# Optimization experiments

Measured on AMD Instinct MI355X. Metric: run time of the kernel, lower is better.

Reference implementation:

```python
import jax, jax.numpy as jnp
import numpy as np

B, T, D, H, C = 32, 512, 1024, 1024, 1000


def setup_inputs() -> dict:
    key = jax.random.key(0)
    ks = jax.random.split(key, 12)
    sc = 0.02
    return {
        "features": jax.random.normal(ks[0], (B, T, D), dtype=jnp.float32),
        "Wp": jax.random.normal(ks[1], (H, D), dtype=jnp.float32) * sc,
        "bp": jnp.zeros((H,), jnp.float32),
        "W_ih": jax.random.normal(ks[2], (3 * H, H), dtype=jnp.float32) * sc,
        "b_ih": jnp.zeros((3 * H,), jnp.float32),
        "W_hh": jax.random.normal(ks[3], (3 * H, H), dtype=jnp.float32) * sc,
        "b_hh": jnp.zeros((3 * H,), jnp.float32),
        "W1": jax.random.normal(ks[4], (H, H), dtype=jnp.float32) * sc,
        "b1": jnp.zeros((H,), jnp.float32),
        "W2": jax.random.normal(ks[5], (C, H), dtype=jnp.float32) * sc,
        "b2": jnp.zeros((C,), jnp.float32),
    }


def _gru_scan(gx, W_hh, b_hh):
    # gx: [B, T, 3H] precomputed input-side gate activations
    def step(h, gx_t):
        gh = h @ W_hh.T + b_hh                  # [B, 3H]
        xr, xz, xn = jnp.split(gx_t, 3, axis=-1)
        hr, hz, hn = jnpp if False else jnp.split(gh, 3, axis=-1)
        r = jax.nn.sigmoid(xr + hr)
        z = jax.nn.sigmoid(xz + hz)
        n = jnp.tanh(xn + r * hn)
        h_new = (1.0 - z) * n + z * h
        return h_new, h_new

    h0 = jnp.zeros((gx.shape[0], W_hh.shape[1]), gx.dtype)
    _, hs = jax.lax.scan(step, h0, jnp.swapaxes(gx, 0, 1))  # [T, B, H]
    return jnp.swapaxes(hs, 0, 1)                            # [B, T, H]


def reference(features, Wp, bp, W_ih, b_ih, W_hh, b_hh, W1, b1, W2, b2):
    # pooled inputs: relu(Linear(features))
    x = jax.nn.relu(jnp.einsum("btd,hd->bth", features, Wp) + bp)  # [B,T,H]
    # input-side gate GEMM batched over all timesteps (the recurrence only
    # needs the hidden-side GEMM per step) -- same math as per-step GRUCell
    gx = jnp.einsum("bth,gh->btg", x, W_ih) + b_ih                 # [B,T,3H]
    hs = _gru_scan(gx, W_hh, b_hh)                                  # [B,T,H]
    out = jax.nn.relu(jnp.einsum("bth,oh->bto", hs, W1) + b1)
    out = jnp.einsum("bth,ch->btc", out, W2) + b2                   # [B,T,C]
    return out
```

## Files before the change

### kernel.cpp

```cpp
#include <hip/hip_runtime.h>
#include <hip/hip_bf16.h>
#include <stdint.h>

#define Bb 32
#define Tt 512
#define Dd 1024
#define Hh 1024
#define Cc 1000
#define Mm (Bb*Tt)
#define SENT 0x7F7F7F7Fu

typedef float f32x4 __attribute__((ext_vector_type(4)));
typedef short bf16x8 __attribute__((ext_vector_type(8)));

#define MFMA16(a,b,c) __builtin_amdgcn_mfma_f32_16x16x32_bf16(a,b,c,0,0,0)

static __device__ __forceinline__ unsigned short f2b(float f){
  __hip_bfloat16 h = __float2bfloat16(f);
  union { __hip_bfloat16 h; unsigned short u; } cv; cv.h = h; return cv.u;
}
static __device__ __forceinline__ float b2f(unsigned short u){
  union { unsigned int i; float f; } cv; cv.i = ((unsigned int)u) << 16; return cv.f;
}

static __device__ __forceinline__ void async16(const ushort* g, ushort* l){
  __builtin_amdgcn_global_load_lds((const __attribute__((address_space(1))) unsigned int*)g,
                                   (__attribute__((address_space(3))) unsigned int*)l,
                                   16, 0, 0);
}

template<int FAST>
static __device__ __forceinline__ bf16x8 h_load(const ushort* p){
  bf16x8 r;
  if constexpr (FAST)
    asm volatile("global_load_dwordx4 %0, %1, off sc1" : "=v"(r) : "v"(p) : "memory");
  else
    asm volatile("global_load_dwordx4 %0, %1, off sc0 sc1" : "=v"(r) : "v"(p) : "memory");
  return r;
}
template<int FAST>
static __device__ __forceinline__ void h_store(ushort* p, unsigned int v){
  if constexpr (FAST)
    asm volatile("global_store_dword %0, %1, off sc1" :: "v"(p), "v"(v) : "memory");
  else
    asm volatile("global_store_dword %0, %1, off sc0 sc1" :: "v"(p), "v"(v) : "memory");
}

static __device__ __forceinline__ int load4sys(const int* p){
  int v;
  asm volatile("global_load_dword %0, %1, off sc0 sc1" : "=v"(v) : "v"(p) : "memory");
  asm volatile("s_waitcnt vmcnt(0)" ::: "memory");
  return v;
}
static __device__ __forceinline__ void store4sys(int* p, int v){
  asm volatile("global_store_dword %0, %1, off sc0 sc1" :: "v"(p), "v"(v) : "memory");
}


__global__ void cvt_bf16(const float* __restrict__ in, ushort* __restrict__ out, int n4){
  int i = blockIdx.x*256 + threadIdx.x;
  if (i < n4){
    const float4 v = ((const float4*)in)[i];
    ushort4 o;
    o.x = f2b(v.x); o.y = f2b(v.y); o.z = f2b(v.z); o.w = f2b(v.w);
    ((ushort4*)out)[i] = o;
  }
}

__global__ void pad_w2(const float* __restrict__ w2, const float* __restrict__ b2,
                       ushort* __restrict__ w2p, float* __restrict__ b2p){
  int i = blockIdx.x*256 + threadIdx.x;
  int r = i >> 10, c = i & 1023;
  w2p[i] = (r < Cc) ? f2b(w2[r*1024 + c]) : (ushort)0;
  if (i < 1024) b2p[i] = (i < Cc) ? b2[i] : 0.f;
}


template<int RELU, int OUT_BF16, int PERM_A, int PERM_C>
__global__ __launch_bounds__(256) void gemm_bt(
    const ushort* __restrict__ A, const ushort* __restrict__ Bm,
    const float* __restrict__ bias, void* __restrict__ Cp,
    int M, int N, int K, int ldc, int nout)
{
  __shared__ ushort As[128*32];
  __shared__ ushort Bs[128*32];
  const int tid  = threadIdx.x;
  const int lane = tid & 63;
  const int wave = tid >> 6;
  const int wr = wave >> 1, wc = wave & 1;
  const int r0 = lane & 15, kg = lane >> 4;

  const int nwg = gridDim.x * gridDim.y;
  const int lin = blockIdx.y * gridDim.x + blockIdx.x;
  const int cpx = nwg >> 3;
  const int swz = (lin & 7) * cpx + (lin >> 3);
  const int bx = swz % gridDim.x, by = swz / gridDim.x;

  const int m0 = bx*128, n0 = by*128;

  const int lrA0 = m0 + (tid>>2);
  const int lrA1 = lrA0 + 64;
  const size_t prA0 = PERM_A ? (size_t)((lrA0 & 511)*32 + (lrA0 >> 9)) : (size_t)lrA0;
  const size_t prA1 = PERM_A ? (size_t)((lrA1 & 511)*32 + (lrA1 >> 9)) : (size_t)lrA1;
  const ushort* aG0 = A  + prA0*K + (tid&3)*8;
  const ushort* aG1 = A  + prA1*K + (tid&3)*8;
  const ushort* bG  = Bm + (size_t)(n0 + (tid>>2))*K + (tid&3)*8;
  ushort* aL = As + tid*8;
  ushort* bL = Bs + tid*8;
  const size_t rstep = (size_t)64*K;

  f32x4 acc[4][4] = {};

  for (int kt = 0; kt < K; kt += 32){
    __syncthreads();
    async16(aG0 + kt, aL);
    async16(aG1 + kt, aL + 2048);
    async16(bG + kt,         bL);
    async16(bG + kt + rstep, bL + 2048);
    __syncthreads();
    bf16x8 af[4], bf_[4];
#pragma unroll
    for (int i=0;i<4;i++) af[i]  = *(const bf16x8*)&As[(wr*64 + i*16 + r0)*32 + kg*8];
#pragma unroll
    for (int j=0;j<4;j++) bf_[j] = *(const bf16x8*)&Bs[(wc*64 + j*16 + r0)*32 + kg*8];
#pragma unroll
    for (int i=0;i<4;i++)
#pragma unroll
      for (int j=0;j<4;j++)
        acc[i][j] = MFMA16(af[i], bf_[j], acc[i][j]);
  }

  const int rowb = m0 + wr*64 + kg*4;
  const int colb = n0 + wc*64 + r0;
#pragma unroll
  for (int i=0;i<4;i++){
#pragma unroll
    for (int j=0;j<4;j++){
      const int c = colb + j*16;
      if (c >= nout) continue;
      const float bv = bias ? bias[c] : 0.f;
#pragma unroll
      for (int q=0;q<4;q++){
        const int r = rowb + i*16 + q;
        const size_t pr = PERM_C ? (size_t)((r & 511)*32 + (r >> 9)) : (size_t)r;
        float v = acc[i][j][q] + bv;
        if (RELU) v = fmaxf(v, 0.f);
        if (OUT_BF16) ((ushort*)Cp)[pr*ldc + c] = f2b(v);
        else          ((float* )Cp)[pr*ldc + c] = v;
      }
    }
  }
}


#define REDN  4656
#define REDN2 1584

template<int FAST>
static __device__ __forceinline__ void scan_body(
    const int g, const int m, const int tid,
    const ushort* __restrict__ Whh, const float* __restrict__ bhh,
    const ushort* __restrict__ W1b, const float* __restrict__ b1,
    const ushort* __restrict__ gxT, ushort* __restrict__ hsAll,
    ushort* __restrict__ o1, float* __restrict__ red, float* __restrict__ red2)
{
  const int wave = tid >> 6;
  const int lane = tid & 63;
  const int r0 = lane & 15, kg = lane >> 4;
  const int kbase = wave*128 + kg*8;

  bf16x8 wb[6][4];
#pragma unroll
  for (int n=0;n<6;n++){
    const ushort* wr_ = Whh + ((size_t)((n>>1)*1024 + m*32 + (n&1)*16 + r0))*1024 + kbase;
#pragma unroll
    for (int ks=0;ks<4;ks++)
      wb[n][ks] = *(const bf16x8*)(wr_ + ks*32);
  }
  bf16x8 w1f[2][4];
#pragma unroll
  for (int n2=0;n2<2;n2++){
    const ushort* wr_ = W1b + ((size_t)(m*32 + n2*16 + r0))*1024 + kbase;
#pragma unroll
    for (int ks=0;ks<4;ks++)
      w1f[n2][ks] = *(const bf16x8*)(wr_ + ks*32);
  }

  const int eb = tid >> 4;
  const int u0 = (tid & 15)*2;
  const int jg = m*32 + u0;
  float br0=0,br1=0,bz0=0,bz1=0,bn0=0,bn1=0;
  if (tid < 64){
    br0 = bhh[jg];       br1 = bhh[jg+1];
    bz0 = bhh[1024+jg];  bz1 = bhh[1024+jg+1];
    bn0 = bhh[2048+jg];  bn1 = bhh[2048+jg+1];
  }
  const int t2  = tid & 63;
  const int eb2 = t2 >> 4;
  const int u02 = (t2 & 15)*2;
  const int jg2 = m*32 + u02;
  float b1a=0, b1b=0;
  if (tid >= 64 && tid < 128){ b1a = b1[jg2]; b1b = b1[jg2+1]; }

  float hold0 = 0.f, hold1 = 0.f;

  unsigned xr=0, xz=0, xn=0, xrN=0, xzN=0, xnN=0;
  if (tid < 64){
    const ushort* gb = gxT + (size_t)(g*4 + eb)*3072 + jg;
    asm volatile("global_load_dword %0, %1, off" : "=v"(xr) : "v"(gb));
    asm volatile("global_load_dword %0, %1, off" : "=v"(xz) : "v"(gb + 1024));
    asm volatile("global_load_dword %0, %1, off" : "=v"(xn) : "v"(gb + 2048));
  }

  bf16x8 ha[4], haP[4];

  for (int t = 0; t <= Tt+1; ++t){
    const int buf = t & 1;
    const int polled = (t <= Tt);

    const ushort* aB = hsAll + (size_t)(t*32 + g*4 + (r0 & 3))*1024 + kbase;
    if (polled){
#pragma unroll
      for (int ks=0;ks<4;ks++) ha[ks] = h_load<FAST>(aB + ks*32);
    }

    if (t >= 2){
      f32x4 acc2[2] = {};
#pragma unroll
      for (int ks=0;ks<4;ks++)
#pragma unroll
        for (int n2=0;n2<2;n2++)
          acc2[n2] = MFMA16(haP[ks], w1f[n2][ks], acc2[n2]);
      if (kg == 0){
        float* rb2 = red2 + buf*REDN2;
#pragma unroll
        for (int n2=0;n2<2;n2++)
#pragma unroll
          for (int q=0;q<4;q++)
            rb2[(q*33 + n2*16 + r0)*12 + wave] = acc2[n2][q];
      }
    }

    if (polled){
      int again;
      for(;;){
        asm volatile("s_waitcnt vmcnt(0)" ::: "memory");
        __builtin_amdgcn_sched_barrier(0);
        unsigned sent = 0;
#pragma unroll
        for (int ks=0;ks<4;ks++){
          union { bf16x8 v; unsigned u[4]; } A; A.v = ha[ks];
#pragma unroll
          for (int q=0;q<4;q++) sent |= (A.u[q] == SENT);
        }
        again = __any((int)sent);
        if (!again) break;
#pragma unroll
        for (int ks=0;ks<4;ks++) ha[ks] = h_load<FAST>(aB + ks*32);
      }
    }

    if (tid < 64 && t+1 < Tt){
      const ushort* gb = gxT + (size_t)((t+1)*32 + g*4 + eb)*3072 + jg;
      asm volatile("global_load_dword %0, %1, off" : "=v"(xrN) : "v"(gb));
      asm volatile("global_load_dword %0, %1, off" : "=v"(xzN) : "v"(gb + 1024));
      asm volatile("global_load_dword %0, %1, off" : "=v"(xnN) : "v"(gb + 2048));
    }

    if (t < Tt){
      f32x4 acc[6] = {};
#pragma unroll
      for (int ks=0;ks<4;ks++)
#pragma unroll
        for (int n=0;n<6;n++)
          acc[n] = MFMA16(ha[ks], wb[n][ks], acc[n]);
      if (kg == 0){
        float* rb = red + buf*REDN;
#pragma unroll
        for (int n=0;n<6;n++)
#pragma unroll
          for (int q=0;q<4;q++)
            rb[(q*97 + n*16 + r0)*12 + wave] = acc[n][q];
      }
    }

    __syncthreads();

    if (t < Tt && tid < 64){
      const float* rb = red + buf*REDN;
      float s[6];
#pragma unroll
      for (int i=0;i<6;i++){
        const int g3 = i >> 1, du = i & 1;
        const int slot = eb*97 + g3*32 + u0 + du;
        const float4 a  = *(const float4*)&rb[slot*12];
        const float4 b4 = *(const float4*)&rb[slot*12 + 4];
        s[i] = (a.x + a.y) + (a.z + a.w) + (b4.x + b4.y) + (b4.z + b4.w);
      }
      float h0, h1;
      {
        const float r = 1.f/(1.f + __expf(-(b2f((ushort)(xr & 0xffff)) + s[0] + br0)));
        const float z = 1.f/(1.f + __expf(-(b2f((ushort)(xz & 0xffff)) + s[2] + bz0)));
        const float a = b2f((ushort)(xn & 0xffff)) + r*(s[4] + bn0);
        const float e = __expf(-2.f*a);
        const float n = (1.f - e)/(1.f + e);
        h0 = (1.f - z)*n + z*hold0; hold0 = h0;
      }
      {
        const float r = 1.f/(1.f + __expf(-(b2f((ushort)(xr >> 16)) + s[1] + br1)));
        const float z = 1.f/(1.f + __expf(-(b2f((ushort)(xz >> 16)) + s[3] + bz1)));
        const float a = b2f((ushort)(xn >> 16)) + r*(s[5] + bn1);
        const float e = __expf(-2.f*a);
        const float n = (1.f - e)/(1.f + e);
        h1 = (1.f - z)*n + z*hold1; hold1 = h1;
      }
      const unsigned packed = (unsigned)f2b(h0) | ((unsigned)f2b(h1) << 16);
      h_store<FAST>(hsAll + (size_t)((t+1)*32 + g*4 + eb)*1024 + jg, packed);
      xr = xrN; xz = xzN; xn = xnN;
    }

    if (t >= 2 && tid >= 64 && tid < 128){
      const float* rb2 = red2 + buf*REDN2;
      float s0, s1;
      {
        const int slot = eb2*33 + u02;
        const float4 a  = *(const float4*)&rb2[slot*12];
        const float4 b4 = *(const float4*)&rb2[slot*12 + 4];
        s0 = (a.x + a.y) + (a.z + a.w) + (b4.x + b4.y) + (b4.z + b4.w);
      }
      {
        const int slot = eb2*33 + u02 + 1;
        const float4 a  = *(const float4*)&rb2[slot*12];
        const float4 b4 = *(const float4*)&rb2[slot*12 + 4];
        s1 = (a.x + a.y) + (a.z + a.w) + (b4.x + b4.y) + (b4.z + b4.w);
      }
      const float o0 = fmaxf(s0 + b1a, 0.f);
      const float o1v = fmaxf(s1 + b1b, 0.f);
      const unsigned packed = (unsigned)f2b(o0) | ((unsigned)f2b(o1v) << 16);
      *(unsigned*)(o1 + (size_t)((t-2)*32 + g*4 + eb2)*1024 + jg2) = packed;
    }

    if (polled){
#pragma unroll
      for (int ks=0;ks<4;ks++) haP[ks] = ha[ks];
    }
  }
}

__global__ __launch_bounds__(512, 1) void gru_scan(
    const ushort* __restrict__ Whh, const float* __restrict__ bhh,
    const ushort* __restrict__ W1b, const float* __restrict__ b1,
    const ushort* __restrict__ gxT,
    ushort* __restrict__ hsAll,
    ushort* __restrict__ o1,
    int* __restrict__ xccTab)
{
  __shared__ float red[2*REDN];
  __shared__ float red2[2*REDN2];
  __shared__ int fastFlag;
  const int bid = blockIdx.x;
  const int g = bid & 7, m = bid >> 3;
  const int tid = threadIdx.x;
  int* decTab = xccTab + 256;

  if (tid == 0){
    int myxcc;
    asm volatile("s_getreg_b32 %0, hwreg(HW_REG_XCC_ID)" : "=s"(myxcc));
    store4sys(&xccTab[bid], myxcc);
    if (m == 0){
      int ok = 1;
      long budget = 200000;
      for (int p = 0; p < 32 && ok; ++p){
        int v;
        do {
          v = load4sys(&xccTab[p*8 + g]);
          if (v == -1){ __builtin_amdgcn_s_sleep(1); if (--budget <= 0){ ok = 0; break; } }
        } while (v == -1);
        if (v != myxcc) ok = 0;
      }
      store4sys(&decTab[g], ok);
      fastFlag = ok;
    } else {
      int v;
      do {
        v = load4sys(&decTab[g]);
        if (v == -1) __builtin_amdgcn_s_sleep(1);
      } while (v == -1);
      fastFlag = v;
    }
  }
  __syncthreads();

  if (fastFlag) scan_body<1>(g, m, tid, Whh, bhh, W1b, b1, gxT, hsAll, o1, red, red2);
  else          scan_body<0>(g, m, tid, Whh, bhh, W1b, b1, gxT, hsAll, o1, red, red2);
}


extern "C" void kernel_launch(void* const* d_in, const int* in_sizes, int n_in,
                              void* d_out, int out_size, void* d_ws, size_t ws_size,
                              hipStream_t stream)
{
  const float* features = (const float*)d_in[0];
  const float* Wp  = (const float*)d_in[1];
  const float* bp  = (const float*)d_in[2];
  const float* Wih = (const float*)d_in[3];
  const float* bih = (const float*)d_in[4];
  const float* Whh = (const float*)d_in[5];
  const float* bhh = (const float*)d_in[6];
  const float* W1  = (const float*)d_in[7];
  const float* b1  = (const float*)d_in[8];
  const float* W2  = (const float*)d_in[9];
  const float* b2  = (const float*)d_in[10];
  float* out = (float*)d_out;

  char* w = (char*)d_ws;
  auto alloc = [&](size_t bytes){ char* p = w; w += (bytes + 255) & ~(size_t)255; return p; };
  ushort* fb    = (ushort*)alloc((size_t)Mm*Dd*2);
  ushort* xb    = (ushort*)alloc((size_t)Mm*Hh*2);
  ushort* gxT   = (ushort*)alloc((size_t)Mm*3*Hh*2);
  ushort* hsAll = (ushort*)alloc((size_t)(Tt+1)*Bb*Hh*2);
  ushort* o1    = (ushort*)alloc((size_t)Mm*Hh*2);
  ushort* wpb   = (ushort*)alloc((size_t)Hh*Dd*2);
  ushort* wihb  = (ushort*)alloc((size_t)3*Hh*Hh*2);
  ushort* whhb  = (ushort*)alloc((size_t)3*Hh*Hh*2);
  ushort* w1b   = (ushort*)alloc((size_t)Hh*Hh*2);
  ushort* w2b   = (ushort*)alloc((size_t)1024*Hh*2);
  float*  b2p   = (float*)alloc(1024*4);
  int*    xccTab= (int*)alloc(264*4);

  hipMemsetAsync(hsAll, 0x7F, (size_t)(Tt+1)*Bb*Hh*2, stream);
  hipMemsetAsync(hsAll, 0x00, (size_t)Bb*Hh*2, stream);
  hipMemsetAsync(xccTab, 0xFF, 264*4, stream);

  auto cvt = [&](const float* src, ushort* dst, size_t n){
    int n4 = (int)(n/4);
    hipLaunchKernelGGL(cvt_bf16, dim3((n4+255)/256), dim3(256), 0, stream, src, dst, n4);
  };
  cvt(features, fb, (size_t)Mm*Dd);
  cvt(Wp,  wpb,  (size_t)Hh*Dd);
  cvt(Wih, wihb, (size_t)3*Hh*Hh);
  cvt(Whh, whhb, (size_t)3*Hh*Hh);
  cvt(W1,  w1b,  (size_t)Hh*Hh);
  hipLaunchKernelGGL(pad_w2, dim3((1024*1024)/256), dim3(256), 0, stream, W2, b2, w2b, b2p);

  hipLaunchKernelGGL((gemm_bt<1,1,0,0>), dim3(Mm/128, Hh/128), dim3(256), 0, stream,
                     fb, wpb, bp, (void*)xb, Mm, Hh, Dd, Hh, Hh);
  hipLaunchKernelGGL((gemm_bt<0,1,0,1>), dim3(Mm/128, (3*Hh)/128), dim3(256), 0, stream,
                     xb, wihb, bih, (void*)gxT, Mm, 3*Hh, Hh, 3*Hh, 3*Hh);

  hipLaunchKernelGGL(gru_scan, dim3(256), dim3(512), 0, stream,
                     whhb, bhh, w1b, b1, gxT, hsAll, o1, xccTab);

  hipLaunchKernelGGL((gemm_bt<0,0,1,0>), dim3(Mm/128, 1024/128), dim3(256), 0, stream,
                     o1, w2b, b2p, (void*)out, Mm, 1024, Hh, Cc, Cc);
}
```

Baseline: 1.882 ms.

## Spread GRU gate epilogue over 128 threads and fuse weight conversion kernels

Replaces five separate weight-conversion launches and the W2 padding kernel with one combined prep_weights kernel, which removes launch overhead. In the recurrent scan, the per-step gate nonlinearity and the W1 epilogue now run on 128 threads with one hidden unit each instead of 64 threads with two, and neighbour values are paired with a lane shuffle before the packed store. This shortens the serial epilogue on the recurrence critical path. It adds a shuffle and an explicit vmcnt wait for the prefetched gate inputs inside the step.

```diff
diff --git a/kernel.cpp b/kernel.cpp
--- a/kernel.cpp
+++ b/kernel.cpp
@@ -67,12 +67,42 @@
   }
 }
 
-__global__ void pad_w2(const float* __restrict__ w2, const float* __restrict__ b2,
-                       ushort* __restrict__ w2p, float* __restrict__ b2p){
-  int i = blockIdx.x*256 + threadIdx.x;
-  int r = i >> 10, c = i & 1023;
-  w2p[i] = (r < Cc) ? f2b(w2[r*1024 + c]) : (ushort)0;
-  if (i < 1024) b2p[i] = (i < Cc) ? b2[i] : 0.f;
+static __device__ __forceinline__ void cvt4(const float* s, ushort* d){
+  const float4 v = *(const float4*)s;
+  ushort4 o; o.x=f2b(v.x); o.y=f2b(v.y); o.z=f2b(v.z); o.w=f2b(v.w);
+  *(ushort4*)d = o;
+}
+__global__ void prep_weights(const float* __restrict__ Wp,  const float* __restrict__ Wih,
+                             const float* __restrict__ Whh, const float* __restrict__ W1,
+                             const float* __restrict__ W2,  const float* __restrict__ b2,
+                             ushort* __restrict__ wpb, ushort* __restrict__ wihb,
+                             ushort* __restrict__ whhb, ushort* __restrict__ w1b,
+                             ushort* __restrict__ w2b, float* __restrict__ b2p)
+{
+  const long i = (long)blockIdx.x*256 + threadIdx.x;
+  const long Q0 = 262144;
+  const long Q1 = Q0 + 786432;
+  const long Q2 = Q1 + 786432;
+  const long Q3 = Q2 + 262144;
+  const long Q4 = Q3 + 262144;
+  const long Q5 = Q4 + 256;
+  if (i < Q0){            cvt4(Wp  + i*4,      wpb  + i*4); }
+  else if (i < Q1){ long j=i-Q0; cvt4(Wih + j*4, wihb + j*4); }
+  else if (i < Q2){ long j=i-Q1; cvt4(Whh + j*4, whhb + j*4); }
+  else if (i < Q3){ long j=i-Q2; cvt4(W1  + j*4, w1b  + j*4); }
+  else if (i < Q4){
+    long j=i-Q3; int r = (int)(j>>8), c4 = (int)(j&255)*4;
+    ushort4 o;
+    if (r < Cc){
+      const float4 v = *(const float4*)&W2[(size_t)r*1024 + c4];
+      o.x=f2b(v.x); o.y=f2b(v.y); o.z=f2b(v.z); o.w=f2b(v.w);
+    } else { o.x=0; o.y=0; o.z=0; o.w=0; }
+    *(ushort4*)&w2b[(size_t)r*1024 + c4] = o;
+  } else if (i < Q5){
+    long j=i-Q4; int c4=(int)j*4;
+#pragma unroll
+    for (int k=0;k<4;k++){ int c=c4+k; b2p[c] = (c<Cc)? b2[c] : 0.f; }
+  }
 }
 
 
@@ -186,27 +216,26 @@
       w1f[n2][ks] = *(const bf16x8*)(wr_ + ks*32);
   }
 
-  const int eb = tid >> 4;
-  const int u0 = (tid & 15)*2;
-  const int jg = m*32 + u0;
-  float br0=0,br1=0,bz0=0,bz1=0,bn0=0,bn1=0;
-  if (tid < 64){
-    br0 = bhh[jg];       br1 = bhh[jg+1];
-    bz0 = bhh[1024+jg];  bz1 = bhh[1024+jg+1];
-    bn0 = bhh[2048+jg];  bn1 = bhh[2048+jg+1];
-  }
-  const int t2  = tid & 63;
-  const int eb2 = t2 >> 4;
-  const int u02 = (t2 & 15)*2;
-  const int jg2 = m*32 + u02;
-  float b1a=0, b1b=0;
-  if (tid >= 64 && tid < 128){ b1a = b1[jg2]; b1b = b1[jg2+1]; }
-
-  float hold0 = 0.f, hold1 = 0.f;
+  const int eb = (tid >> 5) & 3;
+  const int u  = tid & 31;
+  const int jg = m*32 + u;
+  float brg=0, bzg=0, bng=0;
+  if (tid < 128){
+    brg = bhh[jg]; bzg = bhh[1024+jg]; bng = bhh[2048+jg];
+  }
+  const int t3  = tid & 127;
+  const int eb3 = t3 >> 5;
+  const int u3  = t3 & 31;
+  const int jg3 = m*32 + u3;
+  float b1v = 0.f;
+  if (tid >= 128 && tid < 256) b1v = b1[jg3];
+
+  float hold = 0.f;
 
   unsigned xr=0, xz=0, xn=0, xrN=0, xzN=0, xnN=0;
-  if (tid < 64){
-    const ushort* gb = gxT + (size_t)(g*4 + eb)*3072 + jg;
+  const int jgd = jg & ~1;
+  if (tid < 128){
+    const ushort* gb = gxT + (size_t)(g*4 + eb)*3072 + jgd;
     asm volatile("global_load_dword %0, %1, off" : "=v"(xr) : "v"(gb));
     asm volatile("global_load_dword %0, %1, off" : "=v"(xz) : "v"(gb + 1024));
     asm volatile("global_load_dword %0, %1, off" : "=v"(xn) : "v"(gb + 2048));
@@ -260,8 +289,8 @@
       }
     }
 
-    if (tid < 64 && t+1 < Tt){
-      const ushort* gb = gxT + (size_t)((t+1)*32 + g*4 + eb)*3072 + jg;
+    if (tid < 128 && t+1 < Tt){
+      const ushort* gb = gxT + (size_t)((t+1)*32 + g*4 + eb)*3072 + jgd;
       asm volatile("global_load_dword %0, %1, off" : "=v"(xrN) : "v"(gb));
       asm volatile("global_load_dword %0, %1, off" : "=v"(xzN) : "v"(gb + 1024));
       asm volatile("global_load_dword %0, %1, off" : "=v"(xnN) : "v"(gb + 2048));
@@ -286,58 +315,61 @@
 
     __syncthreads();
 
-    if (t < Tt && tid < 64){
+    if (t < Tt && tid < 128){
       const float* rb = red + buf*REDN;
-      float s[6];
-#pragma unroll
-      for (int i=0;i<6;i++){
-        const int g3 = i >> 1, du = i & 1;
-        const int slot = eb*97 + g3*32 + u0 + du;
+      float sr, sz, sn;
+      {
+        const int slot = eb*97 + u;
         const float4 a  = *(const float4*)&rb[slot*12];
         const float4 b4 = *(const float4*)&rb[slot*12 + 4];
-        s[i] = (a.x + a.y) + (a.z + a.w) + (b4.x + b4.y) + (b4.z + b4.w);
-      }
-      float h0, h1;
+        sr = (a.x + a.y) + (a.z + a.w) + (b4.x + b4.y) + (b4.z + b4.w);
+      }
       {
-        const float r = 1.f/(1.f + __expf(-(b2f((ushort)(xr & 0xffff)) + s[0] + br0)));
-        const float z = 1.f/(1.f + __expf(-(b2f((ushort)(xz & 0xffff)) + s[2] + bz0)));
-        const float a = b2f((ushort)(xn & 0xffff)) + r*(s[4] + bn0);
-        const float e = __expf(-2.f*a);
-        const float n = (1.f - e)/(1.f + e);
-        h0 = (1.f - z)*n + z*hold0; hold0 = h0;
+        const int slot = eb*97 + 32 + u;
+        const float4 a  = *(const float4*)&rb[slot*12];
+        const float4 b4 = *(const float4*)&rb[slot*12 + 4];
+        sz = (a.x + a.y) + (a.z + a.w) + (b4.x + b4.y) + (b4.z + b4.w);
       }
       {
-        const float r = 1.f/(1.f + __expf(-(b2f((ushort)(xr >> 16)) + s[1] + br1)));
-        const float z = 1.f/(1.f + __expf(-(b2f((ushort)(xz >> 16)) + s[3] + bz1)));
-        const float a = b2f((ushort)(xn >> 16)) + r*(s[5] + bn1);
-        const float e = __expf(-2.f*a);
-        const float n = (1.f - e)/(1.f + e);
-        h1 = (1.f - z)*n + z*hold1; hold1 = h1;
-      }
-      const unsigned packed = (unsigned)f2b(h0) | ((unsigned)f2b(h1) << 16);
-      h_store<FAST>(hsAll + (size_t)((t+1)*32 + g*4 + eb)*1024 + jg, packed);
+        const int slot = eb*97 + 64 + u;
+        const float4 a  = *(const float4*)&rb[slot*12];
+        const float4 b4 = *(const float4*)&rb[slot*12 + 4];
+        sn = (a.x + a.y) + (a.z + a.w) + (b4.x + b4.y) + (b4.z + b4.w);
+      }
+      const ushort xh = (ushort)((u & 1) ? (xr >> 16) : (xr & 0xffff));
+      const ushort zh = (ushort)((u & 1) ? (xz >> 16) : (xz & 0xffff));
+      const ushort nh = (ushort)((u & 1) ? (xn >> 16) : (xn & 0xffff));
+      const float r = 1.f/(1.f + __expf(-(b2f(xh) + sr + brg)));
+      const float z = 1.f/(1.f + __expf(-(b2f(zh) + sz + bzg)));
+      const float a = b2f(nh) + r*(sn + bng);
+      const float e = __expf(-2.f*a);
+      const float n = (1.f - e)/(1.f + e);
+      const float hnew = (1.f - z)*n + z*hold;
+      hold = hnew;
+      const unsigned hu = (unsigned)f2b(hnew);
+      const unsigned po = (unsigned)__shfl_xor((int)hu, 1);
+      asm volatile("s_waitcnt vmcnt(0)" : "+v"(xrN), "+v"(xzN), "+v"(xnN) :: "memory");
+      __builtin_amdgcn_sched_barrier(0);
       xr = xrN; xz = xzN; xn = xnN;
-    }
-
-    if (t >= 2 && tid >= 64 && tid < 128){
+      if (!(u & 1)){
+        const unsigned packed = hu | (po << 16);
+        h_store<FAST>(hsAll + (size_t)((t+1)*32 + g*4 + eb)*1024 + jg, packed);
+      }
+    }
+
+    if (t >= 2 && tid >= 128 && tid < 256){
       const float* rb2 = red2 + buf*REDN2;
-      float s0, s1;
-      {
-        const int slot = eb2*33 + u02;
-        const float4 a  = *(const float4*)&rb2[slot*12];
-        const float4 b4 = *(const float4*)&rb2[slot*12 + 4];
-        s0 = (a.x + a.y) + (a.z + a.w) + (b4.x + b4.y) + (b4.z + b4.w);
-      }
-      {
-        const int slot = eb2*33 + u02 + 1;
-        const float4 a  = *(const float4*)&rb2[slot*12];
-        const float4 b4 = *(const float4*)&rb2[slot*12 + 4];
-        s1 = (a.x + a.y) + (a.z + a.w) + (b4.x + b4.y) + (b4.z + b4.w);
-      }
-      const float o0 = fmaxf(s0 + b1a, 0.f);
-      const float o1v = fmaxf(s1 + b1b, 0.f);
-      const unsigned packed = (unsigned)f2b(o0) | ((unsigned)f2b(o1v) << 16);
-      *(unsigned*)(o1 + (size_t)((t-2)*32 + g*4 + eb2)*1024 + jg2) = packed;
+      const int slot = eb3*33 + u3;
+      const float4 a  = *(const float4*)&rb2[slot*12];
+      const float4 b4 = *(const float4*)&rb2[slot*12 + 4];
+      const float s0 = (a.x + a.y) + (a.z + a.w) + (b4.x + b4.y) + (b4.z + b4.w);
+      const float o0 = fmaxf(s0 + b1v, 0.f);
+      const unsigned ou = (unsigned)f2b(o0);
+      const unsigned po = (unsigned)__shfl_xor((int)ou, 1);
+      if (!(u3 & 1)){
+        const unsigned packed = ou | (po << 16);
+        *(unsigned*)(o1 + (size_t)((t-2)*32 + g*4 + eb3)*1024 + jg3) = packed;
+      }
     }
 
     if (polled){
@@ -432,16 +464,10 @@
   hipMemsetAsync(hsAll, 0x00, (size_t)Bb*Hh*2, stream);
   hipMemsetAsync(xccTab, 0xFF, 264*4, stream);
 
-  auto cvt = [&](const float* src, ushort* dst, size_t n){
-    int n4 = (int)(n/4);
-    hipLaunchKernelGGL(cvt_bf16, dim3((n4+255)/256), dim3(256), 0, stream, src, dst, n4);
-  };
-  cvt(features, fb, (size_t)Mm*Dd);
-  cvt(Wp,  wpb,  (size_t)Hh*Dd);
-  cvt(Wih, wihb, (size_t)3*Hh*Hh);
-  cvt(Whh, whhb, (size_t)3*Hh*Hh);
-  cvt(W1,  w1b,  (size_t)Hh*Hh);
-  hipLaunchKernelGGL(pad_w2, dim3((1024*1024)/256), dim3(256), 0, stream, W2, b2, w2b, b2p);
+  hipLaunchKernelGGL(cvt_bf16, dim3((Mm*Dd/4 + 255)/256), dim3(256), 0, stream,
+                     features, fb, Mm*Dd/4);
+  hipLaunchKernelGGL(prep_weights, dim3(9217), dim3(256), 0, stream,
+                     Wp, Wih, Whh, W1, W2, b2, wpb, wihb, whhb, w1b, w2b, b2p);
 
   hipLaunchKernelGGL((gemm_bt<1,1,0,0>), dim3(Mm/128, Hh/128), dim3(256), 0, stream,
                      fb, wpb, bp, (void*)xb, Mm, Hh, Dd, Hh, Hh);
```

After: 1.897 ms. About the same (+0.8%).
